# Kernel optimization log

Measured on AMD Instinct MI355X. Metric: run time of the kernel, lower is better.

The kernel has to match this reference:

```python
import jax, jax.numpy as jnp
import numpy as np

PI = jnp.pi

def phasor_encode(x):
    # map phase in [-1,1] to unit complex phasor exp(i*pi*x)
    return jnp.exp(jnp.complex64(1j) * PI * x.astype(jnp.float32))

def phasor_act(z):
    # angle of complex activation, normalized back to [-1,1]
    return jnp.angle(z) / PI

def multi_dense(x, w, b):
    # PhasorMultiDense: x [b,t,d], w [h,d,D], b [h,D] (complex bias, ones init)
    xz = phasor_encode(x)                                      # [b,t,d] complex64
    wz = w.astype(jnp.complex64)
    bz = b.astype(jnp.complex64)
    yz = jnp.einsum('btd,hdD->bhtD', xz, wz) + bz[None, :, None, :]
    return phasor_act(yz)                                      # [b,h,t,D] real

def attend(q, k, v):
    # VSA phasor attention: similarity = Re(qz . conj(kz)) / d, softmax, complex bundle of v phasors
    d = q.shape[-1]
    qz = phasor_encode(q)
    kz = phasor_encode(k)
    scores = jnp.real(jnp.einsum('bhtd,bhTd->bhtT', qz, jnp.conj(kz))) / d
    probs = jax.nn.softmax(scores, axis=-1)
    vz = phasor_encode(v)
    out = jnp.einsum('bhtT,bhTd->bhtd', probs.astype(jnp.complex64), vz)
    return phasor_act(out)                                     # [b,h,t,D]

def setup_inputs() -> dict:
    key = jax.random.key(0)
    ks = jax.random.split(key, 8)
    B, Tq, Tkv, D, H = 2, 1024, 1024, 512, 8
    sw = 1.0 / np.sqrt(D)       # VarianceScaling(1.0) fan_in
    swo = 1.0 / np.sqrt(H * D)
    return {
        'query': jax.random.uniform(ks[0], (B, Tq, D), jnp.float32, -1.0, 1.0),
        'keyvalue': jax.random.uniform(ks[1], (B, Tkv, D), jnp.float32, -1.0, 1.0),
        'wq': jax.random.normal(ks[2], (H, D, D), jnp.float32) * sw,
        'bq': jnp.ones((H, D), jnp.float32),
        'wk': jax.random.normal(ks[3], (H, D, D), jnp.float32) * sw,
        'bk': jnp.ones((H, D), jnp.float32),
        'wv': jax.random.normal(ks[4], (H, D, D), jnp.float32) * sw,
        'bv': jnp.ones((H, D), jnp.float32),
        'wo': jax.random.normal(ks[5], (H * D, D), jnp.float32) * swo,
        'bo': jnp.ones((D,), jnp.float32),
    }

def reference(query, keyvalue, wq, bq, wk, bk, wv, bv, wo, bo):
    q = multi_dense(query, wq, bq)        # [b,h,t,D]
    k = multi_dense(keyvalue, wk, bk)
    v = multi_dense(keyvalue, wv, bv)
    r = attend(q, k, v)                   # [b,h,t,D]
    b_, h_, t_, d_ = r.shape
    r_flat = jnp.transpose(r, (0, 2, 1, 3)).reshape(b_, t_, h_ * d_)  # b t (h d)
    # final PhasorDense
    xz = phasor_encode(r_flat)
    z = jnp.einsum('btd,dD->btD', xz, wo.astype(jnp.complex64)) + bo.astype(jnp.complex64)
    return phasor_act(z)                  # [b, t_q, output_channels]
```

## Files before the change

### kernel.cpp

```cpp
#include <hip/hip_runtime.h>
#include <math.h>


#define PI_F 3.14159274101257324f

typedef __attribute__((ext_vector_type(8))) _Float16 half8;
typedef __attribute__((ext_vector_type(4))) _Float16 half4;
typedef __attribute__((ext_vector_type(2))) _Float16 half2v;
typedef __attribute__((ext_vector_type(16))) float f32x16;
typedef unsigned int u32;

#define MFMA32(a, b, c) __builtin_amdgcn_mfma_f32_32x32x16_f16((a), (b), (c), 0, 0, 0)
#define ROWOF(r, ln) (((r) & 3) + 8 * ((r) >> 2) + 4 * ((ln) >> 5))

__device__ __forceinline__ void gll16(const void* g, void* l) {
    __builtin_amdgcn_global_load_lds(
        (const __attribute__((address_space(1))) u32*)g,
        (__attribute__((address_space(3))) u32*)l, 16, 0, 0);
}

__device__ __forceinline__ void split2(float x, _Float16& h, _Float16& l) {
    _Float16 hh = (_Float16)x;
    h = hh;
    l = (_Float16)((x - (float)hh) * 4096.0f);
}

__device__ __forceinline__ int xcdswz(int bid, int nwg) {
    const int cpx = nwg >> 3;
    return (bid & 7) * cpx + (bid >> 3);
}

#define SLOT 49152

#define ISSUE6(slotoff, kk)                                                  \
    _Pragma("unroll") for (int u_ = 0; u_ < 6; ++u_)                         \
        gll16(sp[u_] + (kk), lds + (slotoff) + dp[u_]);

#define PIPE_WAIT(s, NS)                                                     \
    if ((s) + 3 <= (NS))      asm volatile("s_waitcnt vmcnt(12)" ::: "memory"); \
    else if ((s) + 2 == (NS)) asm volatile("s_waitcnt vmcnt(6)" ::: "memory");  \
    else                      asm volatile("s_waitcnt vmcnt(0)" ::: "memory");  \
    __builtin_amdgcn_s_barrier();                                            \
    __builtin_amdgcn_sched_barrier(0);

#define PIPE_MID(s, NS)                                                      \
    asm volatile("s_waitcnt lgkmcnt(0)" ::: "memory");                       \
    __builtin_amdgcn_sched_barrier(0);                                       \
    __builtin_amdgcn_s_barrier();                                            \
    __builtin_amdgcn_sched_barrier(0);                                       \
    if ((s) + 3 < (NS)) { ISSUE6(off, ((s) + 3) * 64); }

__global__ __launch_bounds__(256) void encode_phasor(
    const float* __restrict__ x,
    _Float16* __restrict__ ch, _Float16* __restrict__ cl,
    _Float16* __restrict__ sh, _Float16* __restrict__ sl)
{
    const int idx = blockIdx.x * 256 + threadIdx.x;
    float4 v = ((const float4*)x)[idx];
    float cc[4], ss[4];
    sincosf(PI_F * v.x, &ss[0], &cc[0]);
    sincosf(PI_F * v.y, &ss[1], &cc[1]);
    sincosf(PI_F * v.z, &ss[2], &cc[2]);
    sincosf(PI_F * v.w, &ss[3], &cc[3]);
    half4 chv, clv, shv, slv;
#pragma unroll
    for (int q = 0; q < 4; ++q) {
        _Float16 a, b;
        split2(cc[q], a, b); chv[q] = a; clv[q] = b;
        split2(ss[q], a, b); shv[q] = a; slv[q] = b;
    }
    ((half4*)ch)[idx] = chv;
    ((half4*)cl)[idx] = clv;
    ((half4*)sh)[idx] = shv;
    ((half4*)sl)[idx] = slv;
}

__global__ __launch_bounds__(256) void tsplit64(
    const float* __restrict__ w, _Float16* __restrict__ th, _Float16* __restrict__ tl,
    int K, int N)
{
    const int kt = blockIdx.x, ntile = blockIdx.y, h = blockIdx.z;
    const int k0 = kt * 64, n0 = ntile * 64;
    __shared__ float T[64][65];
    const int tid = threadIdx.x;
    const float* wb = w + (size_t)h * K * N;
    {
        const int r = tid >> 4, c4 = (tid & 15) * 4;
#pragma unroll
        for (int rr = 0; rr < 64; rr += 16) {
            float4 v = *(const float4*)&wb[(size_t)(k0 + rr + r) * N + n0 + c4];
            T[rr + r][c4 + 0] = v.x; T[rr + r][c4 + 1] = v.y;
            T[rr + r][c4 + 2] = v.z; T[rr + r][c4 + 3] = v.w;
        }
    }
    __syncthreads();
    {
        const int n = tid >> 2, kq = (tid & 3) * 16;
        half8 hv[2], lv[2];
#pragma unroll
        for (int q = 0; q < 16; ++q) {
            float f = T[kq + q][n];
            _Float16 hh, ll; split2(f, hh, ll);
            hv[q >> 3][q & 7] = hh; lv[q >> 3][q & 7] = ll;
        }
        _Float16* oh = th + ((size_t)h * N + n0 + n) * K + k0 + kq;
        _Float16* ol = tl + ((size_t)h * N + n0 + n) * K + k0 + kq;
        *(half8*)oh = hv[0]; *(half8*)(oh + 8) = hv[1];
        *(half8*)ol = lv[0]; *(half8*)(ol + 8) = lv[1];
    }
}

__global__ __launch_bounds__(512, 2) void proj_qk(
    const _Float16* __restrict__ qch, const _Float16* __restrict__ qcl,
    const _Float16* __restrict__ qsh, const _Float16* __restrict__ qsl,
    const _Float16* __restrict__ kch, const _Float16* __restrict__ kcl,
    const _Float16* __restrict__ ksh, const _Float16* __restrict__ ksl,
    const _Float16* __restrict__ wqh, const _Float16* __restrict__ wql,
    const _Float16* __restrict__ wkh, const _Float16* __restrict__ wkl,
    const float* __restrict__ bq, const float* __restrict__ bk,
    _Float16* __restrict__ qzh, _Float16* __restrict__ qzl,
    _Float16* __restrict__ kzh, _Float16* __restrict__ kzl,
    int h0, int hcnt)
{
    const int inp = blockIdx.z;
    const _Float16* xch = inp ? kch : qch;
    const _Float16* xcl = inp ? kcl : qcl;
    const _Float16* xsh = inp ? ksh : qsh;
    const _Float16* xsl = inp ? ksl : qsl;
    const _Float16* wth = inp ? wkh : wqh;
    const _Float16* wtl = inp ? wkl : wql;
    const float* bias = inp ? bk : bq;
    _Float16* ozh = inp ? kzh : qzh;
    _Float16* ozl = inp ? kzl : qzl;

    const int m0 = blockIdx.x * 64;
    const int hc = blockIdx.y >> 1;
    const int n0h = (blockIdx.y & 1) * 256;
    __shared__ char lds[147456];
    const int tid = threadIdx.x, wv = tid >> 6, ln = tid & 63;
    const int wr = wv >> 2, wc = wv & 3, lm32 = ln & 31;

    const char* sp[6]; int dp[6];
#pragma unroll
    for (int u = 0; u < 6; ++u) {
        const int g = u * 8 + wv;
        const _Float16 *ph, *pl; int row0, stride; int f;
        if (g < 8)       { f = g;      ph = xch; pl = xcl; row0 = m0; stride = 512; }
        else if (g < 16) { f = g - 8;  ph = xsh; pl = xsl; row0 = m0; stride = 512; }
        else             { f = g - 16;
                           ph = wth + (size_t)hc * 262144;
                           pl = wtl + (size_t)hc * 262144;
                           row0 = n0h; stride = 512; }
        const int R = f >> 2, ks = (f >> 1) & 1, hl = f & 1;
        sp[u] = (const char*)((hl ? pl : ph)
                + (size_t)(row0 + R * 32 + (ln & 31)) * stride
                + ks * 16 + (ln >> 5) * 8);
        dp[u] = u * 8192 + tid * 16;
    }

    f32x16 ach[2] = {}, acl[2] = {}, ash[2] = {}, asl[2] = {};

    ISSUE6(0, 0); ISSUE6(SLOT, 64); ISSUE6(2 * SLOT, 128);
    int off = 0;
    const int NS = 16;
    for (int s = 0; s < NS; ++s) {
        PIPE_WAIT(s, NS);
        half8 xc[2][2], xs[2][2], w[2][2][2];
#pragma unroll
        for (int ks = 0; ks < 2; ++ks)
#pragma unroll
            for (int hl = 0; hl < 2; ++hl) {
                xc[ks][hl] = *(const half8*)(lds + off + (wr * 4 + ks * 2 + hl) * 1024 + ln * 16);
                xs[ks][hl] = *(const half8*)(lds + off + 8192 + (wr * 4 + ks * 2 + hl) * 1024 + ln * 16);
#pragma unroll
                for (int j = 0; j < 2; ++j)
                    w[ks][j][hl] = *(const half8*)(lds + off + 16384
                        + ((wc * 2 + j) * 4 + ks * 2 + hl) * 1024 + ln * 16);
            }
        PIPE_MID(s, NS);
        __builtin_amdgcn_s_setprio(1);
#pragma unroll
        for (int ks = 0; ks < 2; ++ks)
#pragma unroll
            for (int j = 0; j < 2; ++j) {
                ach[j] = MFMA32(xc[ks][0], w[ks][j][0], ach[j]);
                acl[j] = MFMA32(xc[ks][0], w[ks][j][1], acl[j]);
                acl[j] = MFMA32(xc[ks][1], w[ks][j][0], acl[j]);
                ash[j] = MFMA32(xs[ks][0], w[ks][j][0], ash[j]);
                asl[j] = MFMA32(xs[ks][0], w[ks][j][1], asl[j]);
                asl[j] = MFMA32(xs[ks][1], w[ks][j][0], asl[j]);
            }
        __builtin_amdgcn_s_setprio(0);
        off = (off == 2 * SLOT) ? 0 : off + SLOT;
    }

    const float LS = 1.0f / 4096.0f;
    const int b = m0 >> 10, tbase = m0 & 1023;
    const size_t zz = (size_t)(b * hcnt + hc);
#pragma unroll
    for (int j = 0; j < 2; ++j) {
        const int nloc = wc * 64 + j * 32 + lm32;
        const float bval = bias[(size_t)(h0 + hc) * 512 + n0h + nloc];
#pragma unroll
        for (int r = 0; r < 16; ++r) {
            const int mloc = wr * 32 + ROWOF(r, ln);
            float yc = ach[j][r] + acl[j][r] * LS + bval;
            float ys = ash[j][r] + asl[j][r] * LS;
            float inv = 1.0f / sqrtf(fmaxf(yc * yc + ys * ys, 1e-36f));
            float c = yc * inv, sn = ys * inv;
            _Float16 chh, chl, shh, shl;
            split2(c, chh, chl); split2(sn, shh, shl);
            const size_t offo = (zz * 1024 + tbase + mloc) * 1024 + 2 * (n0h + nloc);
            half2v hv, lv;
            hv[0] = chh; hv[1] = shh; lv[0] = chl; lv[1] = shl;
            *(half2v*)(ozh + offo) = hv;
            *(half2v*)(ozl + offo) = lv;
        }
    }
}

__global__ __launch_bounds__(512, 2) void proj_v(
    const _Float16* __restrict__ xch, const _Float16* __restrict__ xcl,
    const _Float16* __restrict__ xsh, const _Float16* __restrict__ xsl,
    const _Float16* __restrict__ wth, const _Float16* __restrict__ wtl,
    const float* __restrict__ bias,
    _Float16* __restrict__ vch, _Float16* __restrict__ vcl,
    _Float16* __restrict__ vsh, _Float16* __restrict__ vsl,
    int h0, int hcnt)
{
    const int m0 = blockIdx.x * 64;
    const int hc = blockIdx.y >> 1;
    const int n0h = (blockIdx.y & 1) * 256;
    __shared__ char lds[147456];
    const int tid = threadIdx.x, wv = tid >> 6, ln = tid & 63;
    const int wr = wv >> 2, wc = wv & 3, lm32 = ln & 31;

    const char* sp[6]; int dp[6];
#pragma unroll
    for (int u = 0; u < 6; ++u) {
        const int g = u * 8 + wv;
        const _Float16 *ph, *pl; int row0, stride; int f;
        if (g < 8)       { f = g;      ph = xch; pl = xcl; row0 = m0; stride = 512; }
        else if (g < 16) { f = g - 8;  ph = xsh; pl = xsl; row0 = m0; stride = 512; }
        else             { f = g - 16;
                           ph = wth + (size_t)hc * 262144;
                           pl = wtl + (size_t)hc * 262144;
                           row0 = n0h; stride = 512; }
        const int R = f >> 2, ks = (f >> 1) & 1, hl = f & 1;
        sp[u] = (const char*)((hl ? pl : ph)
                + (size_t)(row0 + R * 32 + (ln & 31)) * stride
                + ks * 16 + (ln >> 5) * 8);
        dp[u] = u * 8192 + tid * 16;
    }

    f32x16 ach[2] = {}, acl[2] = {}, ash[2] = {}, asl[2] = {};

    ISSUE6(0, 0); ISSUE6(SLOT, 64); ISSUE6(2 * SLOT, 128);
    int off = 0;
    const int NS = 16;
    for (int s = 0; s < NS; ++s) {
        PIPE_WAIT(s, NS);
        half8 xc[2][2], xs[2][2], w[2][2][2];
#pragma unroll
        for (int ks = 0; ks < 2; ++ks)
#pragma unroll
            for (int hl = 0; hl < 2; ++hl) {
                xc[ks][hl] = *(const half8*)(lds + off + (wr * 4 + ks * 2 + hl) * 1024 + ln * 16);
                xs[ks][hl] = *(const half8*)(lds + off + 8192 + (wr * 4 + ks * 2 + hl) * 1024 + ln * 16);
#pragma unroll
                for (int j = 0; j < 2; ++j)
                    w[ks][j][hl] = *(const half8*)(lds + off + 16384
                        + ((wc * 2 + j) * 4 + ks * 2 + hl) * 1024 + ln * 16);
            }
        PIPE_MID(s, NS);
        __builtin_amdgcn_s_setprio(1);
#pragma unroll
        for (int ks = 0; ks < 2; ++ks)
#pragma unroll
            for (int j = 0; j < 2; ++j) {
                ach[j] = MFMA32(xc[ks][0], w[ks][j][0], ach[j]);
                acl[j] = MFMA32(xc[ks][0], w[ks][j][1], acl[j]);
                acl[j] = MFMA32(xc[ks][1], w[ks][j][0], acl[j]);
                ash[j] = MFMA32(xs[ks][0], w[ks][j][0], ash[j]);
                asl[j] = MFMA32(xs[ks][0], w[ks][j][1], asl[j]);
                asl[j] = MFMA32(xs[ks][1], w[ks][j][0], asl[j]);
            }
        __builtin_amdgcn_s_setprio(0);
        off = (off == 2 * SLOT) ? 0 : off + SLOT;
    }

    const float LS = 1.0f / 4096.0f;
    const int b = m0 >> 10, tbase = m0 & 1023;
    const size_t zz = (size_t)(b * hcnt + hc);
    __syncthreads();
#pragma unroll
    for (int j = 0; j < 2; ++j) {
        const int dloc = wc * 64 + j * 32 + lm32;
        const float bval = bias[(size_t)(h0 + hc) * 512 + n0h + dloc];
#pragma unroll
        for (int r = 0; r < 16; ++r) {
            const int tloc = wr * 32 + ROWOF(r, ln);
            float yc = ach[j][r] + acl[j][r] * LS + bval;
            float ys = ash[j][r] + asl[j][r] * LS;
            float inv = 1.0f / sqrtf(fmaxf(yc * yc + ys * ys, 1e-36f));
            float c = yc * inv, sn = ys * inv;
            _Float16 chh, chl, shh, shl;
            split2(c, chh, chl); split2(sn, shh, shl);
            ((_Float16*)(lds +      0))[dloc * 72 + tloc] = chh;
            ((_Float16*)(lds +  36864))[dloc * 72 + tloc] = chl;
            ((_Float16*)(lds +  73728))[dloc * 72 + tloc] = shh;
            ((_Float16*)(lds + 110592))[dloc * 72 + tloc] = shl;
        }
    }
    __syncthreads();
    {
        const int p = tid >> 7;
        _Float16* outp = (p == 0) ? vch : (p == 1) ? vcl : (p == 2) ? vsh : vsl;
        const int dl = (tid & 127) * 2;
#pragma unroll
        for (int dd = 0; dd < 2; ++dd) {
            const _Float16* srcT = (const _Float16*)(lds + p * 36864) + (dl + dd) * 72;
            _Float16* dst = outp + (zz * 512 + n0h + dl + dd) * 1024 + tbase;
#pragma unroll
            for (int q = 0; q < 8; ++q)
                *(half8*)(dst + q * 8) = *(const half8*)(srcT + q * 8);
        }
    }
}

__global__ __launch_bounds__(512, 2) void scores_mfma(
    const _Float16* __restrict__ qzh, const _Float16* __restrict__ qzl,
    const _Float16* __restrict__ kzh, const _Float16* __restrict__ kzl,
    float* __restrict__ S, int Z)
{
    const int wg = xcdswz(blockIdx.x, Z * 32);
    const int z = wg >> 5;
    const int rem = wg & 31;
    const int m0 = (rem & 7) << 7, n0 = (rem >> 3) << 8;
    __shared__ char lds[147456];
    const size_t zb = (size_t)z << 20;
    const int tid = threadIdx.x, wv = tid >> 6, ln = tid & 63;
    const int wr = wv >> 2, wc = wv & 3, lm32 = ln & 31;

    const char* sp[6]; int dp[6];
#pragma unroll
    for (int u = 0; u < 6; ++u) {
        const int g = u * 8 + wv;
        const _Float16 *ph, *pl; int row0; int f;
        if (g < 16) { f = g;      ph = qzh + zb; pl = qzl + zb; row0 = m0; }
        else        { f = g - 16; ph = kzh + zb; pl = kzl + zb; row0 = n0; }
        const int R = f >> 2, ks = (f >> 1) & 1, hl = f & 1;
        sp[u] = (const char*)((hl ? pl : ph)
                + (size_t)(row0 + R * 32 + (ln & 31)) * 1024
                + ks * 16 + (ln >> 5) * 8);
        dp[u] = u * 8192 + tid * 16;
    }

    f32x16 acch[2][2] = {}, accl[2][2] = {};

    ISSUE6(0, 0); ISSUE6(SLOT, 64); ISSUE6(2 * SLOT, 128);
    int off = 0;
    const int NS = 32;
    for (int s = 0; s < NS; ++s) {
        PIPE_WAIT(s, NS);
        half8 ah[2][2], al[2][2], bh[2][2], bl[2][2];
#pragma unroll
        for (int ks = 0; ks < 2; ++ks)
#pragma unroll
            for (int i = 0; i < 2; ++i) {
                const int Ra = (wr * 2 + i) * 4 + ks * 2;
                ah[ks][i] = *(const half8*)(lds + off + Ra * 1024 + ln * 16);
                al[ks][i] = *(const half8*)(lds + off + (Ra + 1) * 1024 + ln * 16);
                const int Rb = (wc * 2 + i) * 4 + ks * 2;
                bh[ks][i] = *(const half8*)(lds + off + 16384 + Rb * 1024 + ln * 16);
                bl[ks][i] = *(const half8*)(lds + off + 16384 + (Rb + 1) * 1024 + ln * 16);
            }
        PIPE_MID(s, NS);
        __builtin_amdgcn_s_setprio(1);
#pragma unroll
        for (int ks = 0; ks < 2; ++ks)
#pragma unroll
            for (int i = 0; i < 2; ++i)
#pragma unroll
                for (int j = 0; j < 2; ++j) {
                    acch[i][j] = MFMA32(ah[ks][i], bh[ks][j], acch[i][j]);
                    accl[i][j] = MFMA32(ah[ks][i], bl[ks][j], accl[i][j]);
                    accl[i][j] = MFMA32(al[ks][i], bh[ks][j], accl[i][j]);
                }
        __builtin_amdgcn_s_setprio(0);
        off = (off == 2 * SLOT) ? 0 : off + SLOT;
    }
    const float LS = 1.0f / 4096.0f, SC = 1.0f / 512.0f;
#pragma unroll
    for (int i = 0; i < 2; ++i)
#pragma unroll
        for (int j = 0; j < 2; ++j)
#pragma unroll
            for (int r = 0; r < 16; ++r) {
                const int row = m0 + wr * 64 + i * 32 + ROWOF(r, ln);
                const int col = n0 + wc * 64 + j * 32 + lm32;
                S[zb + (size_t)row * 1024 + col] =
                    (acch[i][j][r] + accl[i][j][r] * LS) * SC;
            }
}

__global__ __launch_bounds__(256) void softmax_split(float* __restrict__ S)
{
    const size_t row = blockIdx.x;
    float* p = S + row * 1024;
    const int tid = threadIdx.x;
    float4 v = ((const float4*)p)[tid];
    float m = fmaxf(fmaxf(v.x, v.y), fmaxf(v.z, v.w));
#pragma unroll
    for (int off = 32; off >= 1; off >>= 1)
        m = fmaxf(m, __shfl_xor(m, off));
    __shared__ float redm[4], reds[4];
    const int wid = tid >> 6, lane = tid & 63;
    if (lane == 0) redm[wid] = m;
    __syncthreads();
    m = fmaxf(fmaxf(redm[0], redm[1]), fmaxf(redm[2], redm[3]));
    float4 e;
    e.x = expf(v.x - m); e.y = expf(v.y - m);
    e.z = expf(v.z - m); e.w = expf(v.w - m);
    float s = (e.x + e.y) + (e.z + e.w);
#pragma unroll
    for (int off = 32; off >= 1; off >>= 1)
        s += __shfl_xor(s, off);
    if (lane == 0) reds[wid] = s;
    __syncthreads();
    s = (reds[0] + reds[1]) + (reds[2] + reds[3]);
    e.x /= s; e.y /= s; e.z /= s; e.w /= s;
    __syncthreads();
    _Float16* ph = (_Float16*)p;
    half4 hv, lv;
    _Float16 a, b;
    split2(e.x, a, b); hv[0] = a; lv[0] = b;
    split2(e.y, a, b); hv[1] = a; lv[1] = b;
    split2(e.z, a, b); hv[2] = a; lv[2] = b;
    split2(e.w, a, b); hv[3] = a; lv[3] = b;
    *(half4*)(ph + tid * 4) = hv;
    *(half4*)(ph + 1024 + tid * 4) = lv;
}

__global__ __launch_bounds__(512, 2) void pv_mfma(
    const _Float16* __restrict__ P,
    const _Float16* __restrict__ vch, const _Float16* __restrict__ vcl,
    const _Float16* __restrict__ vsh, const _Float16* __restrict__ vsl,
    _Float16* __restrict__ rch, _Float16* __restrict__ rcl,
    _Float16* __restrict__ rsh, _Float16* __restrict__ rsl,
    int h0, int hcnt, int Z)
{
    const int wg = xcdswz(blockIdx.x, Z * 32);
    const int z = wg >> 5;
    const int rem = wg & 31;
    const int m0 = (rem & 7) << 7, n0 = (rem >> 3) << 7;
    __shared__ char lds[147456];
    const int tid = threadIdx.x, wv = tid >> 6, ln = tid & 63;
    const int wr = wv >> 2, wc = wv & 3, lm32 = ln & 31;

    const _Float16* Pb = P + (size_t)z * 1024 * 2048;
    const size_t vb = (size_t)z * 512 * 1024;
    const char* sp[6]; int dp[6];
#pragma unroll
    for (int u = 0; u < 6; ++u) {
        const int g = u * 8 + wv;
        const _Float16 *ph, *pl; int row0, stride; int f;
        if (g < 16)      { f = g;      ph = Pb; pl = Pb + 1024; row0 = m0; stride = 2048; }
        else if (g < 32) { f = g - 16; ph = vch + vb; pl = vcl + vb; row0 = n0; stride = 1024; }
        else             { f = g - 32; ph = vsh + vb; pl = vsl + vb; row0 = n0; stride = 1024; }
        const int R = f >> 2, ks = (f >> 1) & 1, hl = f & 1;
        sp[u] = (const char*)((hl ? pl : ph)
                + (size_t)(row0 + R * 32 + (ln & 31)) * stride
                + ks * 16 + (ln >> 5) * 8);
        dp[u] = u * 8192 + tid * 16;
    }

    f32x16 ac_h[2] = {}, ac_l[2] = {}, as_h[2] = {}, as_l[2] = {};

    ISSUE6(0, 0); ISSUE6(SLOT, 64); ISSUE6(2 * SLOT, 128);
    int off = 0;
    const int NS = 32;
    for (int s = 0; s < NS; ++s) {
        PIPE_WAIT(s, NS);
        half8 ph_[2][2], pl_[2][2], vc[2][2], vs[2][2];
#pragma unroll
        for (int ks = 0; ks < 2; ++ks) {
#pragma unroll
            for (int i = 0; i < 2; ++i) {
                const int Ra = (wr * 2 + i) * 4 + ks * 2;
                ph_[ks][i] = *(const half8*)(lds + off + Ra * 1024 + ln * 16);
                pl_[ks][i] = *(const half8*)(lds + off + (Ra + 1) * 1024 + ln * 16);
            }
            const int Rv = wc * 4 + ks * 2;
            vc[ks][0] = *(const half8*)(lds + off + 16384 + Rv * 1024 + ln * 16);
            vc[ks][1] = *(const half8*)(lds + off + 16384 + (Rv + 1) * 1024 + ln * 16);
            vs[ks][0] = *(const half8*)(lds + off + 32768 + Rv * 1024 + ln * 16);
            vs[ks][1] = *(const half8*)(lds + off + 32768 + (Rv + 1) * 1024 + ln * 16);
        }
        PIPE_MID(s, NS);
        __builtin_amdgcn_s_setprio(1);
#pragma unroll
        for (int ks = 0; ks < 2; ++ks)
#pragma unroll
            for (int i = 0; i < 2; ++i) {
                ac_h[i] = MFMA32(ph_[ks][i], vc[ks][0], ac_h[i]);
                ac_l[i] = MFMA32(ph_[ks][i], vc[ks][1], ac_l[i]);
                ac_l[i] = MFMA32(pl_[ks][i], vc[ks][0], ac_l[i]);
                as_h[i] = MFMA32(ph_[ks][i], vs[ks][0], as_h[i]);
                as_l[i] = MFMA32(ph_[ks][i], vs[ks][1], as_l[i]);
                as_l[i] = MFMA32(pl_[ks][i], vs[ks][0], as_l[i]);
            }
        __builtin_amdgcn_s_setprio(0);
        off = (off == 2 * SLOT) ? 0 : off + SLOT;
    }
    const float LS = 1.0f / 4096.0f;
    const int b = z / hcnt, hg = h0 + z % hcnt;
#pragma unroll
    for (int i = 0; i < 2; ++i)
#pragma unroll
        for (int r = 0; r < 16; ++r) {
            const int t = m0 + wr * 64 + i * 32 + ROWOF(r, ln);
            const int d = n0 + wc * 32 + lm32;
            float zc = ac_h[i][r] + ac_l[i][r] * LS;
            float zs = as_h[i][r] + as_l[i][r] * LS;
            float inv = 1.0f / sqrtf(fmaxf(zc * zc + zs * zs, 1e-36f));
            float c = zc * inv, sn = zs * inv;
            _Float16 chh, chl, shh, shl;
            split2(c, chh, chl); split2(sn, shh, shl);
            const size_t offo = ((size_t)(b * 1024 + t)) * 4096 + (size_t)hg * 512 + d;
            rch[offo] = chh; rcl[offo] = chl; rsh[offo] = shh; rsl[offo] = shl;
        }
}

__global__ __launch_bounds__(512, 2) void final_mfma(
    const _Float16* __restrict__ rch, const _Float16* __restrict__ rcl,
    const _Float16* __restrict__ rsh, const _Float16* __restrict__ rsl,
    const _Float16* __restrict__ woh, const _Float16* __restrict__ wol,
    float* __restrict__ pbuf)
{
    const int m0 = blockIdx.x * 64, n0 = blockIdx.y * 256;
    const int kspl = blockIdx.z;
    const size_t kbase = (size_t)kspl * 1024;
    __shared__ char lds[147456];
    const int tid = threadIdx.x, wv = tid >> 6, ln = tid & 63;
    const int wr = wv >> 2, wc = wv & 3, lm32 = ln & 31;

    const char* sp[6]; int dp[6];
#pragma unroll
    for (int u = 0; u < 6; ++u) {
        const int g = u * 8 + wv;
        const _Float16 *ph, *pl; int row0; int f;
        if (g < 8)       { f = g;      ph = rch + kbase; pl = rcl + kbase; row0 = m0; }
        else if (g < 16) { f = g - 8;  ph = rsh + kbase; pl = rsl + kbase; row0 = m0; }
        else             { f = g - 16; ph = woh + kbase; pl = wol + kbase; row0 = n0; }
        const int R = f >> 2, ks = (f >> 1) & 1, hl = f & 1;
        sp[u] = (const char*)((hl ? pl : ph)
                + (size_t)(row0 + R * 32 + (ln & 31)) * 4096
                + ks * 16 + (ln >> 5) * 8);
        dp[u] = u * 8192 + tid * 16;
    }

    f32x16 rr_h[2] = {}, rr_l[2] = {}, ri_h[2] = {}, ri_l[2] = {};

    ISSUE6(0, 0); ISSUE6(SLOT, 64); ISSUE6(2 * SLOT, 128);
    int off = 0;
    const int NS = 32;
    for (int s = 0; s < NS; ++s) {
        PIPE_WAIT(s, NS);
        half8 rc[2][2], rs[2][2], w[2][2][2];
#pragma unroll
        for (int ks = 0; ks < 2; ++ks)
#pragma unroll
            for (int hl = 0; hl < 2; ++hl) {
                rc[ks][hl] = *(const half8*)(lds + off + (wr * 4 + ks * 2 + hl) * 1024 + ln * 16);
                rs[ks][hl] = *(const half8*)(lds + off + 8192 + (wr * 4 + ks * 2 + hl) * 1024 + ln * 16);
#pragma unroll
                for (int j = 0; j < 2; ++j)
                    w[ks][j][hl] = *(const half8*)(lds + off + 16384
                        + ((wc * 2 + j) * 4 + ks * 2 + hl) * 1024 + ln * 16);
            }
        PIPE_MID(s, NS);
        __builtin_amdgcn_s_setprio(1);
#pragma unroll
        for (int ks = 0; ks < 2; ++ks)
#pragma unroll
            for (int j = 0; j < 2; ++j) {
                rr_h[j] = MFMA32(rc[ks][0], w[ks][j][0], rr_h[j]);
                rr_l[j] = MFMA32(rc[ks][0], w[ks][j][1], rr_l[j]);
                rr_l[j] = MFMA32(rc[ks][1], w[ks][j][0], rr_l[j]);
                ri_h[j] = MFMA32(rs[ks][0], w[ks][j][0], ri_h[j]);
                ri_l[j] = MFMA32(rs[ks][0], w[ks][j][1], ri_l[j]);
                ri_l[j] = MFMA32(rs[ks][1], w[ks][j][0], ri_l[j]);
            }
        __builtin_amdgcn_s_setprio(0);
        off = (off == 2 * SLOT) ? 0 : off + SLOT;
    }
    const float LS = 1.0f / 4096.0f;
#pragma unroll
    for (int j = 0; j < 2; ++j) {
        const int ng = n0 + wc * 64 + j * 32 + lm32;
#pragma unroll
        for (int r = 0; r < 16; ++r) {
            const int mg = m0 + wr * 32 + ROWOF(r, ln);
            float zr = rr_h[j][r] + rr_l[j][r] * LS;
            float zi = ri_h[j][r] + ri_l[j][r] * LS;
            float2 v; v.x = zr; v.y = zi;
            *(float2*)&pbuf[((size_t)(kspl * 2048 + mg) * 512 + ng) * 2] = v;
        }
    }
}

__global__ __launch_bounds__(256) void final_combine(
    const float* __restrict__ pbuf, const float* __restrict__ bo,
    float* __restrict__ out, int KS)
{
    const int m = blockIdx.x, t = threadIdx.x;
    float4 acc = {0.f, 0.f, 0.f, 0.f};
    for (int s = 0; s < KS; ++s) {
        float4 v = *(const float4*)&pbuf[(size_t)(s * 2048 + m) * 1024 + t * 4];
        acc.x += v.x; acc.y += v.y; acc.z += v.z; acc.w += v.w;
    }
    const int n0 = t * 2;
    out[(size_t)m * 512 + n0]     = atan2f(acc.y, acc.x + bo[n0]) / PI_F;
    out[(size_t)m * 512 + n0 + 1] = atan2f(acc.w, acc.z + bo[n0 + 1]) / PI_F;
}

extern "C" void kernel_launch(void* const* d_in, const int* in_sizes, int n_in,
                              void* d_out, int out_size, void* d_ws, size_t ws_size,
                              hipStream_t stream)
{
    (void)in_sizes; (void)n_in; (void)out_size;
    const float* query    = (const float*)d_in[0];
    const float* keyvalue = (const float*)d_in[1];
    const float* wq = (const float*)d_in[2];
    const float* bq = (const float*)d_in[3];
    const float* wk = (const float*)d_in[4];
    const float* bk = (const float*)d_in[5];
    const float* wv = (const float*)d_in[6];
    const float* bv = (const float*)d_in[7];
    const float* wo = (const float*)d_in[8];
    const float* bo = (const float*)d_in[9];
    float* out = (float*)d_out;

    int hcnt;
    if (ws_size >= (size_t)320 * 1024 * 1024) hcnt = 8;
    else if (ws_size >= (size_t)240 * 1024 * 1024) hcnt = 4;
    else hcnt = 2;
    const int Z = 2 * hcnt;
    const int KS = (hcnt == 2) ? 2 : 4;

    char* p = (char*)d_ws;
    auto alloc = [&](size_t bytes) {
        char* r = p;
        p += (bytes + 255) & ~(size_t)255;
        return r;
    };
    const size_t PLX = (size_t)2048 * 512;
    _Float16* xq[4]; for (int i = 0; i < 4; ++i) xq[i] = (_Float16*)alloc(PLX * 2);
    _Float16* xk[4]; for (int i = 0; i < 4; ++i) xk[i] = (_Float16*)alloc(PLX * 2);
    _Float16* woT[2]; for (int i = 0; i < 2; ++i) woT[i] = (_Float16*)alloc((size_t)512 * 4096 * 2);
    const size_t WTE = (size_t)hcnt * 512 * 512;
    _Float16* wqT[2]; for (int i = 0; i < 2; ++i) wqT[i] = (_Float16*)alloc(WTE * 2);
    _Float16* wkT[2]; for (int i = 0; i < 2; ++i) wkT[i] = (_Float16*)alloc(WTE * 2);
    _Float16* wvT[2]; for (int i = 0; i < 2; ++i) wvT[i] = (_Float16*)alloc(WTE * 2);
    const size_t QZE = (size_t)Z * 1024 * 1024;
    _Float16* qz[2]; for (int i = 0; i < 2; ++i) qz[i] = (_Float16*)alloc(QZE * 2);
    _Float16* kz[2]; for (int i = 0; i < 2; ++i) kz[i] = (_Float16*)alloc(QZE * 2);
    float* S = (float*)alloc(QZE * 4);
    const size_t VTE = (size_t)Z * 512 * 1024;
    _Float16* vT[4]; for (int i = 0; i < 4; ++i) vT[i] = (_Float16*)alloc(VTE * 2);
    const size_t RCE = (size_t)2048 * 4096;
    _Float16* rcs[4];
    if (hcnt == 8) {
        for (int i = 0; i < 4; ++i) rcs[i] = (_Float16*)((char*)qz[0] + (size_t)i * RCE * 2);
    } else {
        for (int i = 0; i < 4; ++i) rcs[i] = (_Float16*)alloc(RCE * 2);
    }
    float* pbuf = (float*)kz[0];

    dim3 blk(256), blk5(512);

    encode_phasor<<<1024, blk, 0, stream>>>(query, xq[0], xq[1], xq[2], xq[3]);
    encode_phasor<<<1024, blk, 0, stream>>>(keyvalue, xk[0], xk[1], xk[2], xk[3]);
    tsplit64<<<dim3(64, 8, 1), blk, 0, stream>>>(wo, woT[0], woT[1], 4096, 512);

    for (int c = 0; c < 8 / hcnt; ++c) {
        const int h0 = c * hcnt;
        const float* wqc = wq + (size_t)h0 * 512 * 512;
        const float* wkc = wk + (size_t)h0 * 512 * 512;
        const float* wvc = wv + (size_t)h0 * 512 * 512;
        tsplit64<<<dim3(8, 8, hcnt), blk, 0, stream>>>(wqc, wqT[0], wqT[1], 512, 512);
        tsplit64<<<dim3(8, 8, hcnt), blk, 0, stream>>>(wkc, wkT[0], wkT[1], 512, 512);
        tsplit64<<<dim3(8, 8, hcnt), blk, 0, stream>>>(wvc, wvT[0], wvT[1], 512, 512);

        proj_qk<<<dim3(32, hcnt * 2, 2), blk5, 0, stream>>>(
            xq[0], xq[1], xq[2], xq[3], xk[0], xk[1], xk[2], xk[3],
            wqT[0], wqT[1], wkT[0], wkT[1], bq, bk,
            qz[0], qz[1], kz[0], kz[1], h0, hcnt);
        proj_v<<<dim3(32, hcnt * 2), blk5, 0, stream>>>(
            xk[0], xk[1], xk[2], xk[3], wvT[0], wvT[1], bv,
            vT[0], vT[1], vT[2], vT[3], h0, hcnt);

        scores_mfma<<<dim3(Z * 32), blk5, 0, stream>>>(qz[0], qz[1], kz[0], kz[1], S, Z);
        softmax_split<<<dim3(Z * 1024), blk, 0, stream>>>(S);
        pv_mfma<<<dim3(Z * 32), blk5, 0, stream>>>(
            (const _Float16*)S, vT[0], vT[1], vT[2], vT[3],
            rcs[0], rcs[1], rcs[2], rcs[3], h0, hcnt, Z);
    }

    final_mfma<<<dim3(32, 2, KS), blk5, 0, stream>>>(
        rcs[0], rcs[1], rcs[2], rcs[3], woT[0], woT[1], pbuf);
    final_combine<<<dim3(2048), blk, 0, stream>>>(pbuf, bo, out, KS);
}
```

Measured before the change: 619.6 us.

## Store MFMA operands in fragment-major layout and load A directly from global

Encoders, weight transposes and projection epilogues now write fp16 hi/lo operands in a fragment-ordered layout (feo), so each lane's MFMA A-fragment is one contiguous 16-byte load straight from global memory. Only the B operand is staged through a smaller double-buffered LDS region. All GEMM kernels move from 512-thread blocks with a three-stage 144KB LDS pipeline to 256-thread blocks with 32KB LDS, smaller N tiles and more blocks. The Q/K projection is split into separate launches and softmax writes split hi/lo probabilities. This aims to cut LDS traffic and footprint and raise occupancy, but it drops the deeper async pipeline and relies on the exposure of direct global A loads being hidden.

```diff
diff --git a/kernel.cpp b/kernel.cpp
--- a/kernel.cpp
+++ b/kernel.cpp
@@ -25,30 +25,15 @@
     l = (_Float16)((x - (float)hh) * 4096.0f);
 }
 
+__device__ __forceinline__ size_t feo(int m, int k, int Kd16) {
+    return ((size_t)((m >> 5) * Kd16 + (k >> 4))) * 512
+           + ((m & 31) + 32 * ((k >> 3) & 1)) * 8 + (k & 7);
+}
+
 __device__ __forceinline__ int xcdswz(int bid, int nwg) {
     const int cpx = nwg >> 3;
     return (bid & 7) * cpx + (bid >> 3);
 }
-
-#define SLOT 49152
-
-#define ISSUE6(slotoff, kk)                                                  \
-    _Pragma("unroll") for (int u_ = 0; u_ < 6; ++u_)                         \
-        gll16(sp[u_] + (kk), lds + (slotoff) + dp[u_]);
-
-#define PIPE_WAIT(s, NS)                                                     \
-    if ((s) + 3 <= (NS))      asm volatile("s_waitcnt vmcnt(12)" ::: "memory"); \
-    else if ((s) + 2 == (NS)) asm volatile("s_waitcnt vmcnt(6)" ::: "memory");  \
-    else                      asm volatile("s_waitcnt vmcnt(0)" ::: "memory");  \
-    __builtin_amdgcn_s_barrier();                                            \
-    __builtin_amdgcn_sched_barrier(0);
-
-#define PIPE_MID(s, NS)                                                      \
-    asm volatile("s_waitcnt lgkmcnt(0)" ::: "memory");                       \
-    __builtin_amdgcn_sched_barrier(0);                                       \
-    __builtin_amdgcn_s_barrier();                                            \
-    __builtin_amdgcn_sched_barrier(0);                                       \
-    if ((s) + 3 < (NS)) { ISSUE6(off, ((s) + 3) * 64); }
 
 __global__ __launch_bounds__(256) void encode_phasor(
     const float* __restrict__ x,
@@ -56,6 +41,7 @@
     _Float16* __restrict__ sh, _Float16* __restrict__ sl)
 {
     const int idx = blockIdx.x * 256 + threadIdx.x;
+    const int m = idx >> 7, k4 = (idx & 127) * 4;
     float4 v = ((const float4*)x)[idx];
     float cc[4], ss[4];
     sincosf(PI_F * v.x, &ss[0], &cc[0]);
@@ -69,10 +55,11 @@
         split2(cc[q], a, b); chv[q] = a; clv[q] = b;
         split2(ss[q], a, b); shv[q] = a; slv[q] = b;
     }
-    ((half4*)ch)[idx] = chv;
-    ((half4*)cl)[idx] = clv;
-    ((half4*)sh)[idx] = shv;
-    ((half4*)sl)[idx] = slv;
+    const size_t off = feo(m, k4, 32);
+    *(half4*)(ch + off) = chv;
+    *(half4*)(cl + off) = clv;
+    *(half4*)(sh + off) = shv;
+    *(half4*)(sl + off) = slv;
 }
 
 __global__ __launch_bounds__(256) void tsplit64(
@@ -95,287 +82,228 @@
     }
     __syncthreads();
     {
-        const int n = tid >> 2, kq = (tid & 3) * 16;
+        const int n = n0 + (tid >> 2), kq = k0 + (tid & 3) * 16;
         half8 hv[2], lv[2];
 #pragma unroll
         for (int q = 0; q < 16; ++q) {
-            float f = T[kq + q][n];
+            float f = T[kq - k0 + q][n - n0];
             _Float16 hh, ll; split2(f, hh, ll);
             hv[q >> 3][q & 7] = hh; lv[q >> 3][q & 7] = ll;
         }
-        _Float16* oh = th + ((size_t)h * N + n0 + n) * K + k0 + kq;
-        _Float16* ol = tl + ((size_t)h * N + n0 + n) * K + k0 + kq;
-        *(half8*)oh = hv[0]; *(half8*)(oh + 8) = hv[1];
-        *(half8*)ol = lv[0]; *(half8*)(ol + 8) = lv[1];
-    }
-}
-
-__global__ __launch_bounds__(512, 2) void proj_qk(
-    const _Float16* __restrict__ qch, const _Float16* __restrict__ qcl,
-    const _Float16* __restrict__ qsh, const _Float16* __restrict__ qsl,
-    const _Float16* __restrict__ kch, const _Float16* __restrict__ kcl,
-    const _Float16* __restrict__ ksh, const _Float16* __restrict__ ksl,
-    const _Float16* __restrict__ wqh, const _Float16* __restrict__ wql,
-    const _Float16* __restrict__ wkh, const _Float16* __restrict__ wkl,
-    const float* __restrict__ bq, const float* __restrict__ bk,
-    _Float16* __restrict__ qzh, _Float16* __restrict__ qzl,
-    _Float16* __restrict__ kzh, _Float16* __restrict__ kzl,
-    int h0, int hcnt)
-{
-    const int inp = blockIdx.z;
-    const _Float16* xch = inp ? kch : qch;
-    const _Float16* xcl = inp ? kcl : qcl;
-    const _Float16* xsh = inp ? ksh : qsh;
-    const _Float16* xsl = inp ? ksl : qsl;
-    const _Float16* wth = inp ? wkh : wqh;
-    const _Float16* wtl = inp ? wkl : wql;
-    const float* bias = inp ? bk : bq;
-    _Float16* ozh = inp ? kzh : qzh;
-    _Float16* ozl = inp ? kzl : qzl;
-
-    const int m0 = blockIdx.x * 64;
-    const int hc = blockIdx.y >> 1;
-    const int n0h = (blockIdx.y & 1) * 256;
-    __shared__ char lds[147456];
-    const int tid = threadIdx.x, wv = tid >> 6, ln = tid & 63;
-    const int wr = wv >> 2, wc = wv & 3, lm32 = ln & 31;
-
-    const char* sp[6]; int dp[6];
-#pragma unroll
-    for (int u = 0; u < 6; ++u) {
-        const int g = u * 8 + wv;
-        const _Float16 *ph, *pl; int row0, stride; int f;
-        if (g < 8)       { f = g;      ph = xch; pl = xcl; row0 = m0; stride = 512; }
-        else if (g < 16) { f = g - 8;  ph = xsh; pl = xsl; row0 = m0; stride = 512; }
-        else             { f = g - 16;
-                           ph = wth + (size_t)hc * 262144;
-                           pl = wtl + (size_t)hc * 262144;
-                           row0 = n0h; stride = 512; }
-        const int R = f >> 2, ks = (f >> 1) & 1, hl = f & 1;
-        sp[u] = (const char*)((hl ? pl : ph)
-                + (size_t)(row0 + R * 32 + (ln & 31)) * stride
-                + ks * 16 + (ln >> 5) * 8);
-        dp[u] = u * 8192 + tid * 16;
-    }
-
-    f32x16 ach[2] = {}, acl[2] = {}, ash[2] = {}, asl[2] = {};
-
-    ISSUE6(0, 0); ISSUE6(SLOT, 64); ISSUE6(2 * SLOT, 128);
-    int off = 0;
-    const int NS = 16;
-    for (int s = 0; s < NS; ++s) {
-        PIPE_WAIT(s, NS);
-        half8 xc[2][2], xs[2][2], w[2][2][2];
-#pragma unroll
-        for (int ks = 0; ks < 2; ++ks)
-#pragma unroll
-            for (int hl = 0; hl < 2; ++hl) {
-                xc[ks][hl] = *(const half8*)(lds + off + (wr * 4 + ks * 2 + hl) * 1024 + ln * 16);
-                xs[ks][hl] = *(const half8*)(lds + off + 8192 + (wr * 4 + ks * 2 + hl) * 1024 + ln * 16);
-#pragma unroll
-                for (int j = 0; j < 2; ++j)
-                    w[ks][j][hl] = *(const half8*)(lds + off + 16384
-                        + ((wc * 2 + j) * 4 + ks * 2 + hl) * 1024 + ln * 16);
-            }
-        PIPE_MID(s, NS);
-        __builtin_amdgcn_s_setprio(1);
-#pragma unroll
-        for (int ks = 0; ks < 2; ++ks)
-#pragma unroll
-            for (int j = 0; j < 2; ++j) {
-                ach[j] = MFMA32(xc[ks][0], w[ks][j][0], ach[j]);
-                acl[j] = MFMA32(xc[ks][0], w[ks][j][1], acl[j]);
-                acl[j] = MFMA32(xc[ks][1], w[ks][j][0], acl[j]);
-                ash[j] = MFMA32(xs[ks][0], w[ks][j][0], ash[j]);
-                asl[j] = MFMA32(xs[ks][0], w[ks][j][1], asl[j]);
-                asl[j] = MFMA32(xs[ks][1], w[ks][j][0], asl[j]);
-            }
-        __builtin_amdgcn_s_setprio(0);
-        off = (off == 2 * SLOT) ? 0 : off + SLOT;
-    }
-
-    const float LS = 1.0f / 4096.0f;
-    const int b = m0 >> 10, tbase = m0 & 1023;
-    const size_t zz = (size_t)(b * hcnt + hc);
-#pragma unroll
-    for (int j = 0; j < 2; ++j) {
-        const int nloc = wc * 64 + j * 32 + lm32;
-        const float bval = bias[(size_t)(h0 + hc) * 512 + n0h + nloc];
-#pragma unroll
-        for (int r = 0; r < 16; ++r) {
-            const int mloc = wr * 32 + ROWOF(r, ln);
-            float yc = ach[j][r] + acl[j][r] * LS + bval;
-            float ys = ash[j][r] + asl[j][r] * LS;
-            float inv = 1.0f / sqrtf(fmaxf(yc * yc + ys * ys, 1e-36f));
-            float c = yc * inv, sn = ys * inv;
-            _Float16 chh, chl, shh, shl;
-            split2(c, chh, chl); split2(sn, shh, shl);
-            const size_t offo = (zz * 1024 + tbase + mloc) * 1024 + 2 * (n0h + nloc);
-            half2v hv, lv;
-            hv[0] = chh; hv[1] = shh; lv[0] = chl; lv[1] = shl;
-            *(half2v*)(ozh + offo) = hv;
-            *(half2v*)(ozl + offo) = lv;
-        }
-    }
-}
-
-__global__ __launch_bounds__(512, 2) void proj_v(
+        const size_t hb = (size_t)h * 512 * K;
+        const size_t offA = hb + ((size_t)((n >> 5) * (K >> 4) + (kq >> 4))) * 512
+                            + (n & 31) * 8;
+        *(half8*)(th + offA) = hv[0]; *(half8*)(th + offA + 256) = hv[1];
+        *(half8*)(tl + offA) = lv[0]; *(half8*)(tl + offA + 256) = lv[1];
+    }
+}
+
+template<bool VT>
+__global__ __launch_bounds__(256, 2) void proj_mfma(
     const _Float16* __restrict__ xch, const _Float16* __restrict__ xcl,
     const _Float16* __restrict__ xsh, const _Float16* __restrict__ xsl,
     const _Float16* __restrict__ wth, const _Float16* __restrict__ wtl,
     const float* __restrict__ bias,
-    _Float16* __restrict__ vch, _Float16* __restrict__ vcl,
-    _Float16* __restrict__ vsh, _Float16* __restrict__ vsl,
+    _Float16* __restrict__ ozh, _Float16* __restrict__ ozl,
+    _Float16* __restrict__ vc_h, _Float16* __restrict__ vc_l,
+    _Float16* __restrict__ vs_h, _Float16* __restrict__ vs_l,
     int h0, int hcnt)
 {
     const int m0 = blockIdx.x * 64;
-    const int hc = blockIdx.y >> 1;
-    const int n0h = (blockIdx.y & 1) * 256;
-    __shared__ char lds[147456];
+    const int hc = blockIdx.y >> 2;
+    const int n0 = (blockIdx.y & 3) * 128;
+    __shared__ char lds[32768];
     const int tid = threadIdx.x, wv = tid >> 6, ln = tid & 63;
-    const int wr = wv >> 2, wc = wv & 3, lm32 = ln & 31;
-
-    const char* sp[6]; int dp[6];
-#pragma unroll
-    for (int u = 0; u < 6; ++u) {
-        const int g = u * 8 + wv;
-        const _Float16 *ph, *pl; int row0, stride; int f;
-        if (g < 8)       { f = g;      ph = xch; pl = xcl; row0 = m0; stride = 512; }
-        else if (g < 16) { f = g - 8;  ph = xsh; pl = xsl; row0 = m0; stride = 512; }
-        else             { f = g - 16;
-                           ph = wth + (size_t)hc * 262144;
-                           pl = wtl + (size_t)hc * 262144;
-                           row0 = n0h; stride = 512; }
-        const int R = f >> 2, ks = (f >> 1) & 1, hl = f & 1;
-        sp[u] = (const char*)((hl ? pl : ph)
-                + (size_t)(row0 + R * 32 + (ln & 31)) * stride
-                + ks * 16 + (ln >> 5) * 8);
-        dp[u] = u * 8192 + tid * 16;
+    const int wr = wv >> 1, wc = wv & 1, lm32 = ln & 31;
+
+    const size_t abase = ((size_t)((m0 >> 5) + wr)) * 32 * 512 + ln * 8;
+    const _Float16* pxc[2] = { xch + abase, xcl + abase };
+    const _Float16* pxs[2] = { xsh + abase, xsl + abase };
+
+    const char* spB[4]; int dpB[4];
+#pragma unroll
+    for (int u = 0; u < 4; ++u) {
+        const int g = wv * 4 + u;
+        const int jt = g >> 2, hl = (g >> 1) & 1, ks = g & 1;
+        const _Float16* base = (hl ? wtl : wth) + (size_t)hc * 262144;
+        spB[u] = (const char*)(base
+                 + ((size_t)(((n0 + jt * 32) >> 5) * 32 + ks)) * 512 + ln * 8);
+        dpB[u] = g * 1024;
     }
 
     f32x16 ach[2] = {}, acl[2] = {}, ash[2] = {}, asl[2] = {};
 
-    ISSUE6(0, 0); ISSUE6(SLOT, 64); ISSUE6(2 * SLOT, 128);
-    int off = 0;
+    auto LOADA = [&](int s, half8 (&ac)[2][2], half8 (&as)[2][2]) {
+#pragma unroll
+        for (int hl = 0; hl < 2; ++hl)
+#pragma unroll
+            for (int ks = 0; ks < 2; ++ks) {
+                ac[hl][ks] = *(const half8*)(pxc[hl] + (2 * s + ks) * 512);
+                as[hl][ks] = *(const half8*)(pxs[hl] + (2 * s + ks) * 512);
+            }
+    };
+    auto STAGEB = [&](int s, int buf) {
+#pragma unroll
+        for (int u = 0; u < 4; ++u)
+            gll16(spB[u] + (size_t)s * 2048, lds + buf + dpB[u]);
+    };
+    auto MSTEP = [&](int buf, half8 (&ac)[2][2], half8 (&as)[2][2]) {
+        half8 w0[2][2], w1[2][2];
+#pragma unroll
+        for (int ks = 0; ks < 2; ++ks)
+#pragma unroll
+            for (int j = 0; j < 2; ++j) {
+                const int gb = (wc * 2 + j) * 4 + ks;
+                w0[ks][j] = *(const half8*)(lds + buf + gb * 1024 + ln * 16);
+                w1[ks][j] = *(const half8*)(lds + buf + (gb + 2) * 1024 + ln * 16);
+            }
+        __builtin_amdgcn_s_setprio(1);
+#pragma unroll
+        for (int ks = 0; ks < 2; ++ks)
+#pragma unroll
+            for (int j = 0; j < 2; ++j) {
+                ach[j] = MFMA32(ac[0][ks], w0[ks][j], ach[j]);
+                acl[j] = MFMA32(ac[0][ks], w1[ks][j], acl[j]);
+                acl[j] = MFMA32(ac[1][ks], w0[ks][j], acl[j]);
+                ash[j] = MFMA32(as[0][ks], w0[ks][j], ash[j]);
+                asl[j] = MFMA32(as[0][ks], w1[ks][j], asl[j]);
+                asl[j] = MFMA32(as[1][ks], w0[ks][j], asl[j]);
+            }
+        __builtin_amdgcn_s_setprio(0);
+    };
+
+    half8 Ac0[2][2], As0[2][2], Ac1[2][2], As1[2][2];
+    LOADA(0, Ac0, As0); STAGEB(0, 0);
     const int NS = 16;
-    for (int s = 0; s < NS; ++s) {
-        PIPE_WAIT(s, NS);
-        half8 xc[2][2], xs[2][2], w[2][2][2];
-#pragma unroll
-        for (int ks = 0; ks < 2; ++ks)
-#pragma unroll
-            for (int hl = 0; hl < 2; ++hl) {
-                xc[ks][hl] = *(const half8*)(lds + off + (wr * 4 + ks * 2 + hl) * 1024 + ln * 16);
-                xs[ks][hl] = *(const half8*)(lds + off + 8192 + (wr * 4 + ks * 2 + hl) * 1024 + ln * 16);
-#pragma unroll
-                for (int j = 0; j < 2; ++j)
-                    w[ks][j][hl] = *(const half8*)(lds + off + 16384
-                        + ((wc * 2 + j) * 4 + ks * 2 + hl) * 1024 + ln * 16);
-            }
-        PIPE_MID(s, NS);
-        __builtin_amdgcn_s_setprio(1);
-#pragma unroll
-        for (int ks = 0; ks < 2; ++ks)
-#pragma unroll
-            for (int j = 0; j < 2; ++j) {
-                ach[j] = MFMA32(xc[ks][0], w[ks][j][0], ach[j]);
-                acl[j] = MFMA32(xc[ks][0], w[ks][j][1], acl[j]);
-                acl[j] = MFMA32(xc[ks][1], w[ks][j][0], acl[j]);
-                ash[j] = MFMA32(xs[ks][0], w[ks][j][0], ash[j]);
-                asl[j] = MFMA32(xs[ks][0], w[ks][j][1], asl[j]);
-                asl[j] = MFMA32(xs[ks][1], w[ks][j][0], asl[j]);
-            }
-        __builtin_amdgcn_s_setprio(0);
-        off = (off == 2 * SLOT) ? 0 : off + SLOT;
+    for (int s = 0; s < NS; s += 2) {
+        __syncthreads();
+        STAGEB(s + 1, 16384); LOADA(s + 1, Ac1, As1);
+        MSTEP(0, Ac0, As0);
+        __syncthreads();
+        if (s + 2 < NS) { STAGEB(s + 2, 0); LOADA(s + 2, Ac0, As0); }
+        MSTEP(16384, Ac1, As1);
     }
 
     const float LS = 1.0f / 4096.0f;
     const int b = m0 >> 10, tbase = m0 & 1023;
     const size_t zz = (size_t)(b * hcnt + hc);
-    __syncthreads();
-#pragma unroll
-    for (int j = 0; j < 2; ++j) {
-        const int dloc = wc * 64 + j * 32 + lm32;
-        const float bval = bias[(size_t)(h0 + hc) * 512 + n0h + dloc];
-#pragma unroll
-        for (int r = 0; r < 16; ++r) {
-            const int tloc = wr * 32 + ROWOF(r, ln);
-            float yc = ach[j][r] + acl[j][r] * LS + bval;
-            float ys = ash[j][r] + asl[j][r] * LS;
-            float inv = 1.0f / sqrtf(fmaxf(yc * yc + ys * ys, 1e-36f));
-            float c = yc * inv, sn = ys * inv;
-            _Float16 chh, chl, shh, shl;
-            split2(c, chh, chl); split2(sn, shh, shl);
-            ((_Float16*)(lds +      0))[dloc * 72 + tloc] = chh;
-            ((_Float16*)(lds +  36864))[dloc * 72 + tloc] = chl;
-            ((_Float16*)(lds +  73728))[dloc * 72 + tloc] = shh;
-            ((_Float16*)(lds + 110592))[dloc * 72 + tloc] = shl;
+    if constexpr (!VT) {
+        const size_t zb = zz << 20;
+#pragma unroll
+        for (int j = 0; j < 2; ++j) {
+            const int nloc = wc * 64 + j * 32 + lm32;
+            const float bval = bias[(size_t)(h0 + hc) * 512 + n0 + nloc];
+            const int kk = 2 * (n0 + nloc);
+#pragma unroll
+            for (int r = 0; r < 16; ++r) {
+                const int mloc = wr * 32 + ROWOF(r, ln);
+                float yc = ach[j][r] + acl[j][r] * LS + bval;
+                float ys = ash[j][r] + asl[j][r] * LS;
+                float inv = 1.0f / sqrtf(fmaxf(yc * yc + ys * ys, 1e-36f));
+                float c = yc * inv, sn = ys * inv;
+                _Float16 chh, chl, shh, shl;
+                split2(c, chh, chl); split2(sn, shh, shl);
+                const size_t off = zb + feo(tbase + mloc, kk, 64);
+                half2v hv, lv;
+                hv[0] = chh; hv[1] = shh; lv[0] = chl; lv[1] = shl;
+                *(half2v*)(ozh + off) = hv;
+                *(half2v*)(ozl + off) = lv;
+            }
         }
-    }
-    __syncthreads();
-    {
-        const int p = tid >> 7;
-        _Float16* outp = (p == 0) ? vch : (p == 1) ? vcl : (p == 2) ? vsh : vsl;
-        const int dl = (tid & 127) * 2;
-#pragma unroll
-        for (int dd = 0; dd < 2; ++dd) {
-            const _Float16* srcT = (const _Float16*)(lds + p * 36864) + (dl + dd) * 72;
-            _Float16* dst = outp + (zz * 512 + n0h + dl + dd) * 1024 + tbase;
-#pragma unroll
-            for (int q = 0; q < 8; ++q)
-                *(half8*)(dst + q * 8) = *(const half8*)(srcT + q * 8);
+    } else {
+        _Float16 vh[4][2][16];
+#pragma unroll
+        for (int j = 0; j < 2; ++j) {
+            const int nloc = wc * 64 + j * 32 + lm32;
+            const float bval = bias[(size_t)(h0 + hc) * 512 + n0 + nloc];
+#pragma unroll
+            for (int r = 0; r < 16; ++r) {
+                float yc = ach[j][r] + acl[j][r] * LS + bval;
+                float ys = ash[j][r] + asl[j][r] * LS;
+                float inv = 1.0f / sqrtf(fmaxf(yc * yc + ys * ys, 1e-36f));
+                _Float16 a, bq_;
+                split2(yc * inv, a, bq_); vh[0][j][r] = a; vh[1][j][r] = bq_;
+                split2(ys * inv, a, bq_); vh[2][j][r] = a; vh[3][j][r] = bq_;
+            }
         }
-    }
-}
-
-__global__ __launch_bounds__(512, 2) void scores_mfma(
+        const size_t zvb = zz * 524288;
+        _Float16* outp[4] = { vc_h, vc_l, vs_h, vs_l };
+#pragma unroll
+        for (int p = 0; p < 4; ++p) {
+            __syncthreads();
+            _Float16* T = (_Float16*)lds;
+#pragma unroll
+            for (int j = 0; j < 2; ++j) {
+                const int dloc = wc * 64 + j * 32 + lm32;
+#pragma unroll
+                for (int r = 0; r < 16; ++r)
+                    T[dloc * 72 + wr * 32 + ROWOF(r, ln)] = vh[p][j][r];
+            }
+            __syncthreads();
+            const int d_l = tid >> 1, seg = tid & 1;
+            const int dg = n0 + d_l;
+#pragma unroll
+            for (int q = 0; q < 4; ++q) {
+                const int tg = tbase + seg * 32 + q * 8;
+                const size_t off = zvb + feo(dg, tg, 64);
+                *(half8*)(outp[p] + off) = *(const half8*)(T + d_l * 72 + seg * 32 + q * 8);
+            }
+        }
+    }
+}
+
+__global__ __launch_bounds__(256, 2) void scores_mfma(
     const _Float16* __restrict__ qzh, const _Float16* __restrict__ qzl,
     const _Float16* __restrict__ kzh, const _Float16* __restrict__ kzl,
     float* __restrict__ S, int Z)
 {
-    const int wg = xcdswz(blockIdx.x, Z * 32);
-    const int z = wg >> 5;
-    const int rem = wg & 31;
-    const int m0 = (rem & 7) << 7, n0 = (rem >> 3) << 8;
-    __shared__ char lds[147456];
+    const int wg = xcdswz(blockIdx.x, Z * 64);
+    const int z = wg >> 6;
+    const int rem = wg & 63;
+    const int m0 = (rem & 7) << 7, n0 = (rem >> 3) << 7;
+    __shared__ char lds[32768];
     const size_t zb = (size_t)z << 20;
     const int tid = threadIdx.x, wv = tid >> 6, ln = tid & 63;
-    const int wr = wv >> 2, wc = wv & 3, lm32 = ln & 31;
-
-    const char* sp[6]; int dp[6];
-#pragma unroll
-    for (int u = 0; u < 6; ++u) {
-        const int g = u * 8 + wv;
-        const _Float16 *ph, *pl; int row0; int f;
-        if (g < 16) { f = g;      ph = qzh + zb; pl = qzl + zb; row0 = m0; }
-        else        { f = g - 16; ph = kzh + zb; pl = kzl + zb; row0 = n0; }
-        const int R = f >> 2, ks = (f >> 1) & 1, hl = f & 1;
-        sp[u] = (const char*)((hl ? pl : ph)
-                + (size_t)(row0 + R * 32 + (ln & 31)) * 1024
-                + ks * 16 + (ln >> 5) * 8);
-        dp[u] = u * 8192 + tid * 16;
+    const int wr = wv >> 1, wc = wv & 1, lm32 = ln & 31;
+
+    const _Float16* pa[2] = { qzh + zb + ln * 8, qzl + zb + ln * 8 };
+    const char* spB[4]; int dpB[4];
+#pragma unroll
+    for (int u = 0; u < 4; ++u) {
+        const int g = wv * 4 + u;
+        const int jt = g >> 2, hl = (g >> 1) & 1, ks = g & 1;
+        spB[u] = (const char*)((hl ? kzl : kzh) + zb
+                 + ((size_t)(((n0 + jt * 32) >> 5) * 64 + ks)) * 512 + ln * 8);
+        dpB[u] = g * 1024;
     }
 
     f32x16 acch[2][2] = {}, accl[2][2] = {};
 
-    ISSUE6(0, 0); ISSUE6(SLOT, 64); ISSUE6(2 * SLOT, 128);
-    int off = 0;
-    const int NS = 32;
-    for (int s = 0; s < NS; ++s) {
-        PIPE_WAIT(s, NS);
-        half8 ah[2][2], al[2][2], bh[2][2], bl[2][2];
+    auto LOADA = [&](int s, half8 (&a)[2][2][2]) {
+#pragma unroll
+        for (int hl = 0; hl < 2; ++hl)
+#pragma unroll
+            for (int i = 0; i < 2; ++i)
+#pragma unroll
+                for (int ks = 0; ks < 2; ++ks)
+                    a[hl][i][ks] = *(const half8*)(pa[hl]
+                        + ((size_t)((m0 >> 5) + wr * 2 + i) * 64 + 2 * s + ks) * 512);
+    };
+    auto STAGEB = [&](int s, int buf) {
+#pragma unroll
+        for (int u = 0; u < 4; ++u)
+            gll16(spB[u] + (size_t)s * 2048, lds + buf + dpB[u]);
+    };
+    auto MSTEP = [&](int buf, half8 (&a)[2][2][2]) {
+        half8 bh[2][2], bl[2][2];
 #pragma unroll
         for (int ks = 0; ks < 2; ++ks)
 #pragma unroll
-            for (int i = 0; i < 2; ++i) {
-                const int Ra = (wr * 2 + i) * 4 + ks * 2;
-                ah[ks][i] = *(const half8*)(lds + off + Ra * 1024 + ln * 16);
-                al[ks][i] = *(const half8*)(lds + off + (Ra + 1) * 1024 + ln * 16);
-                const int Rb = (wc * 2 + i) * 4 + ks * 2;
-                bh[ks][i] = *(const half8*)(lds + off + 16384 + Rb * 1024 + ln * 16);
-                bl[ks][i] = *(const half8*)(lds + off + 16384 + (Rb + 1) * 1024 + ln * 16);
-            }
-        PIPE_MID(s, NS);
+            for (int j = 0; j < 2; ++j) {
+                const int gb = (wc * 2 + j) * 4 + ks;
+                bh[ks][j] = *(const half8*)(lds + buf + gb * 1024 + ln * 16);
+                bl[ks][j] = *(const half8*)(lds + buf + (gb + 2) * 1024 + ln * 16);
+            }
         __builtin_amdgcn_s_setprio(1);
 #pragma unroll
         for (int ks = 0; ks < 2; ++ks)
@@ -383,12 +311,23 @@
             for (int i = 0; i < 2; ++i)
 #pragma unroll
                 for (int j = 0; j < 2; ++j) {
-                    acch[i][j] = MFMA32(ah[ks][i], bh[ks][j], acch[i][j]);
-                    accl[i][j] = MFMA32(ah[ks][i], bl[ks][j], accl[i][j]);
-                    accl[i][j] = MFMA32(al[ks][i], bh[ks][j], accl[i][j]);
+                    acch[i][j] = MFMA32(a[0][i][ks], bh[ks][j], acch[i][j]);
+                    accl[i][j] = MFMA32(a[0][i][ks], bl[ks][j], accl[i][j]);
+                    accl[i][j] = MFMA32(a[1][i][ks], bh[ks][j], accl[i][j]);
                 }
         __builtin_amdgcn_s_setprio(0);
-        off = (off == 2 * SLOT) ? 0 : off + SLOT;
+    };
+
+    half8 A0[2][2][2], A1[2][2][2];
+    LOADA(0, A0); STAGEB(0, 0);
+    const int NS = 32;
+    for (int s = 0; s < NS; s += 2) {
+        __syncthreads();
+        STAGEB(s + 1, 16384); LOADA(s + 1, A1);
+        MSTEP(0, A0);
+        __syncthreads();
+        if (s + 2 < NS) { STAGEB(s + 2, 0); LOADA(s + 2, A0); }
+        MSTEP(16384, A1);
     }
     const float LS = 1.0f / 4096.0f, SC = 1.0f / 512.0f;
 #pragma unroll
@@ -404,10 +343,11 @@
             }
 }
 
-__global__ __launch_bounds__(256) void softmax_split(float* __restrict__ S)
-{
-    const size_t row = blockIdx.x;
-    float* p = S + row * 1024;
+__global__ __launch_bounds__(256) void softmax_split(
+    const float* __restrict__ S, _Float16* __restrict__ Ph, _Float16* __restrict__ Pl)
+{
+    const int z = blockIdx.x >> 10, t = blockIdx.x & 1023;
+    const float* p = S + ((size_t)blockIdx.x << 10);
     const int tid = threadIdx.x;
     float4 v = ((const float4*)p)[tid];
     float m = fmaxf(fmaxf(v.x, v.y), fmaxf(v.z, v.w));
@@ -430,88 +370,97 @@
     __syncthreads();
     s = (reds[0] + reds[1]) + (reds[2] + reds[3]);
     e.x /= s; e.y /= s; e.z /= s; e.w /= s;
-    __syncthreads();
-    _Float16* ph = (_Float16*)p;
     half4 hv, lv;
     _Float16 a, b;
     split2(e.x, a, b); hv[0] = a; lv[0] = b;
     split2(e.y, a, b); hv[1] = a; lv[1] = b;
     split2(e.z, a, b); hv[2] = a; lv[2] = b;
     split2(e.w, a, b); hv[3] = a; lv[3] = b;
-    *(half4*)(ph + tid * 4) = hv;
-    *(half4*)(ph + 1024 + tid * 4) = lv;
-}
-
-__global__ __launch_bounds__(512, 2) void pv_mfma(
-    const _Float16* __restrict__ P,
+    const size_t off = ((size_t)z << 20) + feo(t, tid * 4, 64);
+    *(half4*)(Ph + off) = hv;
+    *(half4*)(Pl + off) = lv;
+}
+
+__global__ __launch_bounds__(256, 2) void pv_mfma(
+    const _Float16* __restrict__ Ph, const _Float16* __restrict__ Pl,
     const _Float16* __restrict__ vch, const _Float16* __restrict__ vcl,
     const _Float16* __restrict__ vsh, const _Float16* __restrict__ vsl,
     _Float16* __restrict__ rch, _Float16* __restrict__ rcl,
     _Float16* __restrict__ rsh, _Float16* __restrict__ rsl,
     int h0, int hcnt, int Z)
 {
-    const int wg = xcdswz(blockIdx.x, Z * 32);
-    const int z = wg >> 5;
-    const int rem = wg & 31;
-    const int m0 = (rem & 7) << 7, n0 = (rem >> 3) << 7;
-    __shared__ char lds[147456];
+    const int wg = xcdswz(blockIdx.x, Z * 64);
+    const int z = wg >> 6;
+    const int rem = wg & 63;
+    const int m0 = (rem & 7) << 7, n0 = (rem >> 3) << 6;
+    __shared__ char lds[32768];
     const int tid = threadIdx.x, wv = tid >> 6, ln = tid & 63;
-    const int wr = wv >> 2, wc = wv & 3, lm32 = ln & 31;
-
-    const _Float16* Pb = P + (size_t)z * 1024 * 2048;
-    const size_t vb = (size_t)z * 512 * 1024;
-    const char* sp[6]; int dp[6];
-#pragma unroll
-    for (int u = 0; u < 6; ++u) {
-        const int g = u * 8 + wv;
-        const _Float16 *ph, *pl; int row0, stride; int f;
-        if (g < 16)      { f = g;      ph = Pb; pl = Pb + 1024; row0 = m0; stride = 2048; }
-        else if (g < 32) { f = g - 16; ph = vch + vb; pl = vcl + vb; row0 = n0; stride = 1024; }
-        else             { f = g - 32; ph = vsh + vb; pl = vsl + vb; row0 = n0; stride = 1024; }
-        const int R = f >> 2, ks = (f >> 1) & 1, hl = f & 1;
-        sp[u] = (const char*)((hl ? pl : ph)
-                + (size_t)(row0 + R * 32 + (ln & 31)) * stride
-                + ks * 16 + (ln >> 5) * 8);
-        dp[u] = u * 8192 + tid * 16;
+    const int wr = wv >> 1, wc = wv & 1, lm32 = ln & 31;
+
+    const size_t zb = (size_t)z << 20, zvb = (size_t)z * 524288;
+    const _Float16* pa[2] = { Ph + zb + ln * 8, Pl + zb + ln * 8 };
+    const char* spB[4]; int dpB[4];
+#pragma unroll
+    for (int u = 0; u < 4; ++u) {
+        const int g = wv * 4 + u;
+        const int pl = g >> 3, dt = (g >> 2) & 1, hl = (g >> 1) & 1, ks = g & 1;
+        const _Float16* base = pl ? (hl ? vsl : vsh) : (hl ? vcl : vch);
+        spB[u] = (const char*)(base + zvb
+                 + ((size_t)(((n0 + dt * 32) >> 5) * 64 + ks)) * 512 + ln * 8);
+        dpB[u] = g * 1024;
     }
 
     f32x16 ac_h[2] = {}, ac_l[2] = {}, as_h[2] = {}, as_l[2] = {};
 
-    ISSUE6(0, 0); ISSUE6(SLOT, 64); ISSUE6(2 * SLOT, 128);
-    int off = 0;
+    auto LOADA = [&](int s, half8 (&a)[2][2][2]) {
+#pragma unroll
+        for (int hl = 0; hl < 2; ++hl)
+#pragma unroll
+            for (int i = 0; i < 2; ++i)
+#pragma unroll
+                for (int ks = 0; ks < 2; ++ks)
+                    a[hl][i][ks] = *(const half8*)(pa[hl]
+                        + ((size_t)((m0 >> 5) + wr * 2 + i) * 64 + 2 * s + ks) * 512);
+    };
+    auto STAGEB = [&](int s, int buf) {
+#pragma unroll
+        for (int u = 0; u < 4; ++u)
+            gll16(spB[u] + (size_t)s * 2048, lds + buf + dpB[u]);
+    };
+    auto MSTEP = [&](int buf, half8 (&a)[2][2][2]) {
+        half8 vc[2][2], vs[2][2];
+#pragma unroll
+        for (int hl = 0; hl < 2; ++hl)
+#pragma unroll
+            for (int ks = 0; ks < 2; ++ks) {
+                vc[hl][ks] = *(const half8*)(lds + buf + (wc * 4 + hl * 2 + ks) * 1024 + ln * 16);
+                vs[hl][ks] = *(const half8*)(lds + buf + (8 + wc * 4 + hl * 2 + ks) * 1024 + ln * 16);
+            }
+        __builtin_amdgcn_s_setprio(1);
+#pragma unroll
+        for (int ks = 0; ks < 2; ++ks)
+#pragma unroll
+            for (int i = 0; i < 2; ++i) {
+                ac_h[i] = MFMA32(a[0][i][ks], vc[0][ks], ac_h[i]);
+                ac_l[i] = MFMA32(a[0][i][ks], vc[1][ks], ac_l[i]);
+                ac_l[i] = MFMA32(a[1][i][ks], vc[0][ks], ac_l[i]);
+                as_h[i] = MFMA32(a[0][i][ks], vs[0][ks], as_h[i]);
+                as_l[i] = MFMA32(a[0][i][ks], vs[1][ks], as_l[i]);
+                as_l[i] = MFMA32(a[1][i][ks], vs[0][ks], as_l[i]);
+            }
+        __builtin_amdgcn_s_setprio(0);
+    };
+
+    half8 A0[2][2][2], A1[2][2][2];
+    LOADA(0, A0); STAGEB(0, 0);
     const int NS = 32;
-    for (int s = 0; s < NS; ++s) {
-        PIPE_WAIT(s, NS);
-        half8 ph_[2][2], pl_[2][2], vc[2][2], vs[2][2];
-#pragma unroll
-        for (int ks = 0; ks < 2; ++ks) {
-#pragma unroll
-            for (int i = 0; i < 2; ++i) {
-                const int Ra = (wr * 2 + i) * 4 + ks * 2;
-                ph_[ks][i] = *(const half8*)(lds + off + Ra * 1024 + ln * 16);
-                pl_[ks][i] = *(const half8*)(lds + off + (Ra + 1) * 1024 + ln * 16);
-            }
-            const int Rv = wc * 4 + ks * 2;
-            vc[ks][0] = *(const half8*)(lds + off + 16384 + Rv * 1024 + ln * 16);
-            vc[ks][1] = *(const half8*)(lds + off + 16384 + (Rv + 1) * 1024 + ln * 16);
-            vs[ks][0] = *(const half8*)(lds + off + 32768 + Rv * 1024 + ln * 16);
-            vs[ks][1] = *(const half8*)(lds + off + 32768 + (Rv + 1) * 1024 + ln * 16);
-        }
-        PIPE_MID(s, NS);
-        __builtin_amdgcn_s_setprio(1);
-#pragma unroll
-        for (int ks = 0; ks < 2; ++ks)
-#pragma unroll
-            for (int i = 0; i < 2; ++i) {
-                ac_h[i] = MFMA32(ph_[ks][i], vc[ks][0], ac_h[i]);
-                ac_l[i] = MFMA32(ph_[ks][i], vc[ks][1], ac_l[i]);
-                ac_l[i] = MFMA32(pl_[ks][i], vc[ks][0], ac_l[i]);
-                as_h[i] = MFMA32(ph_[ks][i], vs[ks][0], as_h[i]);
-                as_l[i] = MFMA32(ph_[ks][i], vs[ks][1], as_l[i]);
-                as_l[i] = MFMA32(pl_[ks][i], vs[ks][0], as_l[i]);
-            }
-        __builtin_amdgcn_s_setprio(0);
-        off = (off == 2 * SLOT) ? 0 : off + SLOT;
+    for (int s = 0; s < NS; s += 2) {
+        __syncthreads();
+        STAGEB(s + 1, 16384); LOADA(s + 1, A1);
+        MSTEP(0, A0);
+        __syncthreads();
+        if (s + 2 < NS) { STAGEB(s + 2, 0); LOADA(s + 2, A0); }
+        MSTEP(16384, A1);
     }
     const float LS = 1.0f / 4096.0f;
     const int b = z / hcnt, hg = h0 + z % hcnt;
@@ -524,76 +473,91 @@
             float zc = ac_h[i][r] + ac_l[i][r] * LS;
             float zs = as_h[i][r] + as_l[i][r] * LS;
             float inv = 1.0f / sqrtf(fmaxf(zc * zc + zs * zs, 1e-36f));
-            float c = zc * inv, sn = zs * inv;
             _Float16 chh, chl, shh, shl;
-            split2(c, chh, chl); split2(sn, shh, shl);
-            const size_t offo = ((size_t)(b * 1024 + t)) * 4096 + (size_t)hg * 512 + d;
-            rch[offo] = chh; rcl[offo] = chl; rsh[offo] = shh; rsl[offo] = shl;
+            split2(zc * inv, chh, chl);
+            split2(zs * inv, shh, shl);
+            const size_t off = feo(b * 1024 + t, hg * 512 + d, 256);
+            rch[off] = chh; rcl[off] = chl; rsh[off] = shh; rsl[off] = shl;
         }
 }
 
-__global__ __launch_bounds__(512, 2) void final_mfma(
+__global__ __launch_bounds__(256, 2) void final_mfma(
     const _Float16* __restrict__ rch, const _Float16* __restrict__ rcl,
     const _Float16* __restrict__ rsh, const _Float16* __restrict__ rsl,
     const _Float16* __restrict__ woh, const _Float16* __restrict__ wol,
     float* __restrict__ pbuf)
 {
-    const int m0 = blockIdx.x * 64, n0 = blockIdx.y * 256;
+    const int m0 = blockIdx.x * 64, n0 = blockIdx.y * 128;
     const int kspl = blockIdx.z;
-    const size_t kbase = (size_t)kspl * 1024;
-    __shared__ char lds[147456];
+    const int kf = kspl * 64;
+    __shared__ char lds[32768];
     const int tid = threadIdx.x, wv = tid >> 6, ln = tid & 63;
-    const int wr = wv >> 2, wc = wv & 3, lm32 = ln & 31;
-
-    const char* sp[6]; int dp[6];
-#pragma unroll
-    for (int u = 0; u < 6; ++u) {
-        const int g = u * 8 + wv;
-        const _Float16 *ph, *pl; int row0; int f;
-        if (g < 8)       { f = g;      ph = rch + kbase; pl = rcl + kbase; row0 = m0; }
-        else if (g < 16) { f = g - 8;  ph = rsh + kbase; pl = rsl + kbase; row0 = m0; }
-        else             { f = g - 16; ph = woh + kbase; pl = wol + kbase; row0 = n0; }
-        const int R = f >> 2, ks = (f >> 1) & 1, hl = f & 1;
-        sp[u] = (const char*)((hl ? pl : ph)
-                + (size_t)(row0 + R * 32 + (ln & 31)) * 4096
-                + ks * 16 + (ln >> 5) * 8);
-        dp[u] = u * 8192 + tid * 16;
+    const int wr = wv >> 1, wc = wv & 1, lm32 = ln & 31;
+
+    const size_t abase = ((size_t)((m0 >> 5) + wr) * 256 + kf) * 512 + ln * 8;
+    const _Float16* prc[2] = { rch + abase, rcl + abase };
+    const _Float16* prs[2] = { rsh + abase, rsl + abase };
+    const char* spB[4]; int dpB[4];
+#pragma unroll
+    for (int u = 0; u < 4; ++u) {
+        const int g = wv * 4 + u;
+        const int jt = g >> 2, hl = (g >> 1) & 1, ks = g & 1;
+        spB[u] = (const char*)((hl ? wol : woh)
+                 + ((size_t)(((n0 + jt * 32) >> 5) * 256 + kf + ks)) * 512 + ln * 8);
+        dpB[u] = g * 1024;
     }
 
     f32x16 rr_h[2] = {}, rr_l[2] = {}, ri_h[2] = {}, ri_l[2] = {};
 
-    ISSUE6(0, 0); ISSUE6(SLOT, 64); ISSUE6(2 * SLOT, 128);
-    int off = 0;
+    auto LOADA = [&](int s, half8 (&ac)[2][2], half8 (&as)[2][2]) {
+#pragma unroll
+        for (int hl = 0; hl < 2; ++hl)
+#pragma unroll
+            for (int ks = 0; ks < 2; ++ks) {
+                ac[hl][ks] = *(const half8*)(prc[hl] + (2 * s + ks) * 512);
+                as[hl][ks] = *(const half8*)(prs[hl] + (2 * s + ks) * 512);
+            }
+    };
+    auto STAGEB = [&](int s, int buf) {
+#pragma unroll
+        for (int u = 0; u < 4; ++u)
+            gll16(spB[u] + (size_t)s * 2048, lds + buf + dpB[u]);
+    };
+    auto MSTEP = [&](int buf, half8 (&ac)[2][2], half8 (&as)[2][2]) {
+        half8 w0[2][2], w1[2][2];
+#pragma unroll
+        for (int ks = 0; ks < 2; ++ks)
+#pragma unroll
+            for (int j = 0; j < 2; ++j) {
+                const int gb = (wc * 2 + j) * 4 + ks;
+                w0[ks][j] = *(const half8*)(lds + buf + gb * 1024 + ln * 16);
+                w1[ks][j] = *(const half8*)(lds + buf + (gb + 2) * 1024 + ln * 16);
+            }
+        __builtin_amdgcn_s_setprio(1);
+#pragma unroll
+        for (int ks = 0; ks < 2; ++ks)
+#pragma unroll
+            for (int j = 0; j < 2; ++j) {
+                rr_h[j] = MFMA32(ac[0][ks], w0[ks][j], rr_h[j]);
+                rr_l[j] = MFMA32(ac[0][ks], w1[ks][j], rr_l[j]);
+                rr_l[j] = MFMA32(ac[1][ks], w0[ks][j], rr_l[j]);
+                ri_h[j] = MFMA32(as[0][ks], w0[ks][j], ri_h[j]);
+                ri_l[j] = MFMA32(as[0][ks], w1[ks][j], ri_l[j]);
+                ri_l[j] = MFMA32(as[1][ks], w0[ks][j], ri_l[j]);
+            }
+        __builtin_amdgcn_s_setprio(0);
+    };
+
+    half8 Ac0[2][2], As0[2][2], Ac1[2][2], As1[2][2];
+    LOADA(0, Ac0, As0); STAGEB(0, 0);
     const int NS = 32;
-    for (int s = 0; s < NS; ++s) {
-        PIPE_WAIT(s, NS);
-        half8 rc[2][2], rs[2][2], w[2][2][2];
-#pragma unroll
-        for (int ks = 0; ks < 2; ++ks)
-#pragma unroll
-            for (int hl = 0; hl < 2; ++hl) {
-                rc[ks][hl] = *(const half8*)(lds + off + (wr * 4 + ks * 2 + hl) * 1024 + ln * 16);
-                rs[ks][hl] = *(const half8*)(lds + off + 8192 + (wr * 4 + ks * 2 + hl) * 1024 + ln * 16);
-#pragma unroll
-                for (int j = 0; j < 2; ++j)
-                    w[ks][j][hl] = *(const half8*)(lds + off + 16384
-                        + ((wc * 2 + j) * 4 + ks * 2 + hl) * 1024 + ln * 16);
-            }
-        PIPE_MID(s, NS);
-        __builtin_amdgcn_s_setprio(1);
-#pragma unroll
-        for (int ks = 0; ks < 2; ++ks)
-#pragma unroll
-            for (int j = 0; j < 2; ++j) {
-                rr_h[j] = MFMA32(rc[ks][0], w[ks][j][0], rr_h[j]);
-                rr_l[j] = MFMA32(rc[ks][0], w[ks][j][1], rr_l[j]);
-                rr_l[j] = MFMA32(rc[ks][1], w[ks][j][0], rr_l[j]);
-                ri_h[j] = MFMA32(rs[ks][0], w[ks][j][0], ri_h[j]);
-                ri_l[j] = MFMA32(rs[ks][0], w[ks][j][1], ri_l[j]);
-                ri_l[j] = MFMA32(rs[ks][1], w[ks][j][0], ri_l[j]);
-            }
-        __builtin_amdgcn_s_setprio(0);
-        off = (off == 2 * SLOT) ? 0 : off + SLOT;
+    for (int s = 0; s < NS; s += 2) {
+        __syncthreads();
+        STAGEB(s + 1, 16384); LOADA(s + 1, Ac1, As1);
+        MSTEP(0, Ac0, As0);
+        __syncthreads();
+        if (s + 2 < NS) { STAGEB(s + 2, 0); LOADA(s + 2, Ac0, As0); }
+        MSTEP(16384, Ac1, As1);
     }
     const float LS = 1.0f / 4096.0f;
 #pragma unroll
@@ -602,9 +566,9 @@
 #pragma unroll
         for (int r = 0; r < 16; ++r) {
             const int mg = m0 + wr * 32 + ROWOF(r, ln);
-            float zr = rr_h[j][r] + rr_l[j][r] * LS;
-            float zi = ri_h[j][r] + ri_l[j][r] * LS;
-            float2 v; v.x = zr; v.y = zi;
+            float2 v;
+            v.x = rr_h[j][r] + rr_l[j][r] * LS;
+            v.y = ri_h[j][r] + ri_l[j][r] * LS;
             *(float2*)&pbuf[((size_t)(kspl * 2048 + mg) * 512 + ng) * 2] = v;
         }
     }
@@ -676,9 +640,11 @@
     } else {
         for (int i = 0; i < 4; ++i) rcs[i] = (_Float16*)alloc(RCE * 2);
     }
+    _Float16* Ph = kz[0];
+    _Float16* Pl = kz[1];
     float* pbuf = (float*)kz[0];
 
-    dim3 blk(256), blk5(512);
+    dim3 blk(256);
 
     encode_phasor<<<1024, blk, 0, stream>>>(query, xq[0], xq[1], xq[2], xq[3]);
     encode_phasor<<<1024, blk, 0, stream>>>(keyvalue, xk[0], xk[1], xk[2], xk[3]);
@@ -693,22 +659,24 @@
         tsplit64<<<dim3(8, 8, hcnt), blk, 0, stream>>>(wkc, wkT[0], wkT[1], 512, 512);
         tsplit64<<<dim3(8, 8, hcnt), blk, 0, stream>>>(wvc, wvT[0], wvT[1], 512, 512);
 
-        proj_qk<<<dim3(32, hcnt * 2, 2), blk5, 0, stream>>>(
-            xq[0], xq[1], xq[2], xq[3], xk[0], xk[1], xk[2], xk[3],
-            wqT[0], wqT[1], wkT[0], wkT[1], bq, bk,
-            qz[0], qz[1], kz[0], kz[1], h0, hcnt);
-        proj_v<<<dim3(32, hcnt * 2), blk5, 0, stream>>>(
+        proj_mfma<false><<<dim3(32, hcnt * 4), blk, 0, stream>>>(
+            xq[0], xq[1], xq[2], xq[3], wqT[0], wqT[1], bq,
+            qz[0], qz[1], nullptr, nullptr, nullptr, nullptr, h0, hcnt);
+        proj_mfma<false><<<dim3(32, hcnt * 4), blk, 0, stream>>>(
+            xk[0], xk[1], xk[2], xk[3], wkT[0], wkT[1], bk,
+            kz[0], kz[1], nullptr, nullptr, nullptr, nullptr, h0, hcnt);
+        proj_mfma<true><<<dim3(32, hcnt * 4), blk, 0, stream>>>(
             xk[0], xk[1], xk[2], xk[3], wvT[0], wvT[1], bv,
-            vT[0], vT[1], vT[2], vT[3], h0, hcnt);
-
-        scores_mfma<<<dim3(Z * 32), blk5, 0, stream>>>(qz[0], qz[1], kz[0], kz[1], S, Z);
-        softmax_split<<<dim3(Z * 1024), blk, 0, stream>>>(S);
-        pv_mfma<<<dim3(Z * 32), blk5, 0, stream>>>(
-            (const _Float16*)S, vT[0], vT[1], vT[2], vT[3],
+            nullptr, nullptr, vT[0], vT[1], vT[2], vT[3], h0, hcnt);
+
+        scores_mfma<<<dim3(Z * 64), blk, 0, stream>>>(qz[0], qz[1], kz[0], kz[1], S, Z);
+        softmax_split<<<dim3(Z * 1024), blk, 0, stream>>>(S, Ph, Pl);
+        pv_mfma<<<dim3(Z * 64), blk, 0, stream>>>(
+            Ph, Pl, vT[0], vT[1], vT[2], vT[3],
             rcs[0], rcs[1], rcs[2], rcs[3], h0, hcnt, Z);
     }
 
-    final_mfma<<<dim3(32, 2, KS), blk5, 0, stream>>>(
+    final_mfma<<<dim3(32, 4, KS), blk, 0, stream>>>(
         rcs[0], rcs[1], rcs[2], rcs[3], woT[0], woT[1], pbuf);
     final_combine<<<dim3(2048), blk, 0, stream>>>(pbuf, bo, out, KS);
 }
```

After: 595.4 us. -3.9%, faster.
